# Kernel tuning notes

Hardware: AMD Instinct MI355X
Metric: run time of the kernel (lower is better)

## Reference

```python
import jax, jax.numpy as jnp
import numpy as np

WS = 8            # window_size
SHIFT = WS // 2   # cyclic shift for 'SW' type
HEAD_DIM = 32

def _rel_index(ws):
    # pairwise relative coordinate indices within a window, offset to [0, 2ws-2]
    cord = np.array([[i, j] for i in range(ws) for j in range(ws)])
    rel = cord[:, None, :] - cord[None, :, :] + ws - 1
    return rel[:, :, 0], rel[:, :, 1]

def _shift_mask(h_w, w_w, p):
    # boolean attention mask for shifted windows; True = masked (-inf)
    s = p - SHIFT
    m = np.zeros((h_w, w_w, p, p, p, p), dtype=bool)
    m[-1, :, :s, :, s:, :] = True
    m[-1, :, s:, :, :s, :] = True
    m[:, -1, :, :s, :, s:] = True
    m[:, -1, :, s:, :, :s] = True
    return m.reshape(h_w * w_w, p * p, p * p)

def setup_inputs() -> dict:
    key = jax.random.key(0)
    ks = jax.random.split(key, 6)
    b, H, W, c = 4, 256, 256, 256
    nh = c // HEAD_DIM
    return {
        "x": jax.random.normal(ks[0], (b, H, W, c), jnp.float32),
        "W_qkv": jax.random.normal(ks[1], (c, 3 * c), jnp.float32) * 0.02,
        "b_qkv": jnp.zeros((3 * c,), jnp.float32),
        "rel_pos": jax.random.normal(ks[2], (nh, 2 * WS - 1, 2 * WS - 1), jnp.float32) * 0.02,
        "W_out": jax.random.normal(ks[3], (c, c), jnp.float32) * 0.02,
        "b_out": jnp.zeros((c,), jnp.float32),
    }

def reference(x, W_qkv, b_qkv, rel_pos, W_out, b_out):
    b, H, W, c = x.shape
    nh = c // HEAD_DIM
    scale = HEAD_DIM ** -0.5
    # cyclic shift (type == 'SW')
    x = jnp.roll(x, (-SHIFT, -SHIFT), axis=(1, 2))
    hw, ww = H // WS, W // WS
    nw, p2 = hw * ww, WS * WS
    # partition into windows: [b, nw, p2, c]
    xw = x.reshape(b, hw, WS, ww, WS, c).transpose(0, 1, 3, 2, 4, 5).reshape(b, nw, p2, c)
    # QKV projection; layout of out dim is (3, n_heads, head_dim)
    qkv = (xw @ W_qkv + b_qkv).reshape(b, nw, p2, 3, nh, HEAD_DIM)
    q, k, v = qkv[..., 0, :, :], qkv[..., 1, :, :], qkv[..., 2, :, :]
    # attention scores per head/window: [h, b, nw, p2, p2]
    sim = jnp.einsum('bwphc,bwqhc->hbwpq', q, k) * scale
    ri, rj = _rel_index(WS)
    sim = sim + rel_pos[:, ri, rj][:, None, None]            # relative position bias
    mask = jnp.asarray(_shift_mask(hw, ww, WS))              # [nw, p2, p2]
    sim = jnp.where(mask[None, None], -jnp.inf, sim)
    probs = jax.nn.softmax(sim, axis=-1)
    out = jnp.einsum('hbwpq,bwqhc->bwphc', probs, v).reshape(b, nw, p2, nh * HEAD_DIM)
    out = out @ W_out + b_out
    # un-window: [b, H, W, c_out]
    out = out.reshape(b, hw, ww, WS, WS, -1).transpose(0, 1, 3, 2, 4, 5).reshape(b, H, W, -1)
    return jnp.roll(out, (SHIFT, SHIFT), axis=(1, 2))
```

## Files before the change

kernel.cpp:

```cpp
#include <hip/hip_runtime.h>
#include <hip/hip_bf16.h>

typedef __attribute__((ext_vector_type(4))) float f32x4;
typedef __attribute__((ext_vector_type(2))) unsigned int u32x2;
typedef __attribute__((ext_vector_type(8))) short s16x8;
typedef __attribute__((ext_vector_type(8))) __bf16 bf16v8;
typedef __attribute__((ext_vector_type(8))) _Float16 f16v8;
typedef __attribute__((ext_vector_type(4))) _Float16 f16x4;

#define LDS_XS 0
#define LDS_QS 32768
#define LDS_KS 65536
#define LDS_VT 98304
#define LDS_TOT 131072

__device__ __forceinline__ f32x4 mfma16(s16x8 a, s16x8 b, f32x4 c) {
  return __builtin_amdgcn_mfma_f32_16x16x32_bf16(
      __builtin_bit_cast(bf16v8, a), __builtin_bit_cast(bf16v8, b), c, 0, 0, 0);
}
__device__ __forceinline__ f32x4 mfma16h(s16x8 a, s16x8 b, f32x4 c) {
  return __builtin_amdgcn_mfma_f32_16x16x32_f16(
      __builtin_bit_cast(f16v8, a), __builtin_bit_cast(f16v8, b), c, 0, 0, 0);
}
__device__ __forceinline__ f32x4 mfmah16(f16x4 a, f16x4 b, f32x4 c) {
  return __builtin_amdgcn_mfma_f32_16x16x16f16(a, b, c, 0, 0, 0);
}

__device__ __forceinline__ unsigned int cvt2(float a, float b) {
  __hip_bfloat162 r = __float22bfloat162_rn(make_float2(a, b));
  unsigned int u;
  __builtin_memcpy(&u, &r, 4);
  return u;
}
__device__ __forceinline__ unsigned int cvt2h(float a, float b) {
  auto r = __builtin_amdgcn_cvt_pkrtz(a, b);
  unsigned int u;
  __builtin_memcpy(&u, &r, 4);
  return u;
}
__device__ __forceinline__ f16x4 pack4h(float a, float b, float c, float d) {
  u32x2 u;
  u.x = cvt2h(a, b);
  u.y = cvt2h(c, d);
  f16x4 r;
  __builtin_memcpy(&r, &u, 8);
  return r;
}

__device__ __forceinline__ short f2bf(float f) {
  unsigned u = __float_as_uint(f);
  u += 0x7fffu + ((u >> 16) & 1u);
  return (short)(u >> 16);
}

__device__ __forceinline__ int swz512(int row, int colByte) {
  return row * 512 + (colByte ^ ((row & 7) << 4));
}
__device__ __forceinline__ int swz128(int row, int colByte) {
  return row * 128 + (colByte ^ ((row & 7) << 4));
}

__global__ void prep_w(const float* __restrict__ Wqkv, const float* __restrict__ Wout,
                       const float* __restrict__ relp,
                       short* __restrict__ wqkvT, short* __restrict__ wH,
                       float* __restrict__ relt) {
  int t = blockIdx.x * 256 + threadIdx.x;
  if (t < 768 * 256) {
    int n = t >> 8, k = t & 255;
    wqkvT[t] = f2bf(Wqkv[k * 768 + n]);
  } else if (t < 768 * 256 + 256 * 256) {
    int t2 = t - 768 * 256;
    int n = t2 >> 8, k = t2 & 255;
    _Float16 h = (_Float16)Wout[k * 256 + n];
    unsigned short us;
    __builtin_memcpy(&us, &h, 2);
    wH[t2] = (short)us;
  } else {
    int u = t - 768 * 256 - 256 * 256;
    int r = u & 3, l = (u >> 2) & 63, strip = (u >> 8) & 3;
    int qt = (u >> 10) & 3, h = (u >> 12) & 7, var = (u >> 15) & 3;
    int p = strip * 16 + (l & 15);
    int q = qt * 16 + ((l >> 4) << 2) + r;
    int pi = p >> 3, pj = p & 7, qi = q >> 3, qj = q & 7;
    bool mrow = (var >> 1) & 1, mcol = var & 1;
    bool mk = (mrow && ((pi < 4) != (qi < 4))) || (mcol && ((pj < 4) != (qj < 4)));
    relt[u] = mk ? -1e30f : relp[h * 225 + (pi - qi + 7) * 15 + (pj - qj + 7)];
  }
}

__global__ __launch_bounds__(1024) void swin_mfma(
    const float* __restrict__ x, const float* __restrict__ bqkv,
    const float* __restrict__ bout,
    const short* __restrict__ wqkvT, const short* __restrict__ wH,
    const float* __restrict__ relt, float* __restrict__ out)
{
  __shared__ __align__(16) char lds[LDS_TOT];

  const int tx = threadIdx.x;
  const int w  = tx >> 6;
  const int l  = tx & 63;
  const int g  = l >> 4;
  const int li = l & 15;

  const int b   = blockIdx.x >> 10;
  const int wdw = blockIdx.x & 1023;
  const int wh  = wdw >> 5, wwi = wdw & 31;

  for (int i = 0; i < 4; ++i) {
    int idx = tx + i * 1024;
    int p = idx >> 6, c4 = idx & 63;
    int pi = p >> 3, pj = p & 7;
    int sr = (wh * 8 + pi + 4) & 255;
    int sc = (wwi * 8 + pj + 4) & 255;
    f32x4 v = *(const f32x4*)(x + ((((size_t)b * 256 + sr) * 256 + sc) * 256 + c4 * 4));
    u32x2 uu;
    uu.x = cvt2(v[0], v[1]);
    uu.y = cvt2(v[2], v[3]);
    *(u32x2*)(lds + LDS_XS + swz512(p, c4 * 8)) = uu;
  }
  __syncthreads();

  {
    f32x4 acc[3][4];
    #pragma unroll
    for (int j = 0; j < 3; ++j)
      #pragma unroll
      for (int rb = 0; rb < 4; ++rb)
        acc[j][rb] = (f32x4){0.f, 0.f, 0.f, 0.f};

    int cb[3];
    #pragma unroll
    for (int j = 0; j < 3; ++j) cb[j] = w * 3 + j;

    s16x8 bcur[3], bnext[3];
    #pragma unroll
    for (int j = 0; j < 3; ++j)
      bcur[j] = *(const s16x8*)(wqkvT + (size_t)(cb[j] * 16 + li) * 256 + g * 8);

    #pragma unroll
    for (int kk = 0; kk < 8; ++kk) {
      s16x8 a[4];
      #pragma unroll
      for (int rb = 0; rb < 4; ++rb)
        a[rb] = *(const s16x8*)(lds + LDS_XS + swz512(rb * 16 + li, kk * 64 + g * 16));
      if (kk < 7) {
        #pragma unroll
        for (int j = 0; j < 3; ++j)
          bnext[j] = *(const s16x8*)(wqkvT + (size_t)(cb[j] * 16 + li) * 256
                                     + (kk + 1) * 32 + g * 8);
      }
      #pragma unroll
      for (int j = 0; j < 3; ++j) {
        if (cb[j] < 32)
          #pragma unroll
          for (int rb = 0; rb < 4; ++rb)
            acc[j][rb] = mfma16(bcur[j], a[rb], acc[j][rb]);
        else
          #pragma unroll
          for (int rb = 0; rb < 4; ++rb)
            acc[j][rb] = mfma16(a[rb], bcur[j], acc[j][rb]);
      }
      if (kk < 7) {
        #pragma unroll
        for (int j = 0; j < 3; ++j) bcur[j] = bnext[j];
      }
    }

    #pragma unroll
    for (int j = 0; j < 3; ++j) {
      const int c = cb[j];
      if (c < 16) {
        f32x4 bq = *(const f32x4*)(bqkv + c * 16 + g * 4);
        #pragma unroll
        for (int rb = 0; rb < 4; ++rb) {
          const float SC = 0.17677669529663687f;
          u32x2 uu;
          uu.x = cvt2((acc[j][rb][0] + bq[0]) * SC, (acc[j][rb][1] + bq[1]) * SC);
          uu.y = cvt2((acc[j][rb][2] + bq[2]) * SC, (acc[j][rb][3] + bq[3]) * SC);
          *(u32x2*)(lds + LDS_QS + swz512(rb * 16 + li, c * 32 + g * 8)) = uu;
        }
      } else if (c < 32) {
        f32x4 bk = *(const f32x4*)(bqkv + c * 16 + g * 4);
        #pragma unroll
        for (int rb = 0; rb < 4; ++rb) {
          u32x2 uu;
          uu.x = cvt2(acc[j][rb][0] + bk[0], acc[j][rb][1] + bk[1]);
          uu.y = cvt2(acc[j][rb][2] + bk[2], acc[j][rb][3] + bk[3]);
          *(u32x2*)(lds + LDS_KS + swz512(rb * 16 + li, (c - 16) * 32 + g * 8)) = uu;
        }
      } else {
        const int d = (c - 32) * 16 + li;
        const float bv = bqkv[c * 16 + li];
        #pragma unroll
        for (int rb = 0; rb < 4; ++rb) {
          u32x2 uu;
          uu.x = cvt2h(acc[j][rb][0] + bv, acc[j][rb][1] + bv);
          uu.y = cvt2h(acc[j][rb][2] + bv, acc[j][rb][3] + bv);
          *(u32x2*)(lds + LDS_VT + swz128(d, rb * 32 + g * 8)) = uu;
        }
      }
    }
  }
  __syncthreads();

  {
    const int rvar = ((wh == 31) ? 2 : 0) | ((wwi == 31) ? 1 : 0);
    const int h = w >> 1, phalf = w & 1, p0 = phalf * 32;

    f32x4 rc[2][4];
    #pragma unroll
    for (int pt = 0; pt < 2; ++pt)
      #pragma unroll
      for (int qt = 0; qt < 4; ++qt)
        rc[pt][qt] = *(const f32x4*)(relt
            + ((((rvar * 8 + h) * 4 + qt) * 4 + (phalf * 2 + pt)) * 64 + l) * 4);

    s16x8 qf[2];
    #pragma unroll
    for (int pt = 0; pt < 2; ++pt)
      qf[pt] = *(const s16x8*)(lds + LDS_QS + swz512(p0 + pt * 16 + li, h * 64 + g * 16));
    s16x8 kf[4];
    #pragma unroll
    for (int qt = 0; qt < 4; ++qt)
      kf[qt] = *(const s16x8*)(lds + LDS_KS + swz512(qt * 16 + li, h * 64 + g * 16));
    f16x4 vf[2][4];
    #pragma unroll
    for (int dt = 0; dt < 2; ++dt)
      #pragma unroll
      for (int qt = 0; qt < 4; ++qt)
        vf[dt][qt] = *(const f16x4*)(lds + LDS_VT
                                     + swz128(h * 32 + dt * 16 + li, qt * 32 + g * 8));

    f32x4 simT[2][4];
    #pragma unroll
    for (int pt = 0; pt < 2; ++pt)
      #pragma unroll
      for (int qt = 0; qt < 4; ++qt)
        simT[pt][qt] = mfma16(kf[qt], qf[pt], rc[pt][qt]);

    float rinv[2];
    f16x4 pa[2][4];
    #pragma unroll
    for (int pt = 0; pt < 2; ++pt) {
      float s = 0.f;
      #pragma unroll
      for (int qt = 0; qt < 4; ++qt) {
        float e0 = __expf(simT[pt][qt][0]);
        float e1 = __expf(simT[pt][qt][1]);
        float e2 = __expf(simT[pt][qt][2]);
        float e3 = __expf(simT[pt][qt][3]);
        s += (e0 + e1) + (e2 + e3);
        pa[pt][qt] = pack4h(e0, e1, e2, e3);
      }
      s += __shfl_xor(s, 16);
      s += __shfl_xor(s, 32);
      rinv[pt] = 1.0f / s;
    }

    f32x4 at[2][2];
    #pragma unroll
    for (int pt = 0; pt < 2; ++pt)
      #pragma unroll
      for (int dt = 0; dt < 2; ++dt)
        at[pt][dt] = (f32x4){0.f, 0.f, 0.f, 0.f};
    #pragma unroll
    for (int qt = 0; qt < 4; ++qt)
      #pragma unroll
      for (int pt = 0; pt < 2; ++pt)
        #pragma unroll
        for (int dt = 0; dt < 2; ++dt)
          at[pt][dt] = mfmah16(vf[dt][qt], pa[pt][qt], at[pt][dt]);

    #pragma unroll
    for (int pt = 0; pt < 2; ++pt)
      #pragma unroll
      for (int dt = 0; dt < 2; ++dt) {
        const f32x4 a4 = at[pt][dt];
        u32x2 hh;
        hh.x = cvt2h(a4[0] * rinv[pt], a4[1] * rinv[pt]);
        hh.y = cvt2h(a4[2] * rinv[pt], a4[3] * rinv[pt]);
        *(u32x2*)(lds + LDS_XS + swz512(p0 + pt * 16 + li, h * 64 + dt * 32 + g * 8)) = hh;
      }
  }
  __syncthreads();

  {
    f32x4 acc2[4];
    #pragma unroll
    for (int rb = 0; rb < 4; ++rb)
      acc2[rb] = (f32x4){0.f, 0.f, 0.f, 0.f};

    s16x8 bc = *(const s16x8*)(wH + (size_t)(w * 16 + li) * 256 + g * 8);
    s16x8 bn;

    #pragma unroll
    for (int kk = 0; kk < 8; ++kk) {
      s16x8 a[4];
      #pragma unroll
      for (int rb = 0; rb < 4; ++rb)
        a[rb] = *(const s16x8*)(lds + LDS_XS + swz512(rb * 16 + li, kk * 64 + g * 16));
      if (kk < 7)
        bn = *(const s16x8*)(wH + (size_t)(w * 16 + li) * 256 + (kk + 1) * 32 + g * 8);
      #pragma unroll
      for (int rb = 0; rb < 4; ++rb)
        acc2[rb] = mfma16h(a[rb], bc, acc2[rb]);
      if (kk < 7) bc = bn;
    }

    const int n = w * 16 + li;
    const float bo = bout[n];
    #pragma unroll
    for (int rb = 0; rb < 4; ++rb)
      #pragma unroll
      for (int r = 0; r < 4; ++r) {
        int m = rb * 16 + g * 4 + r;
        int pi = m >> 3, pj = m & 7;
        int dr = (wh * 8 + pi + 4) & 255;
        int dc = (wwi * 8 + pj + 4) & 255;
        out[(((size_t)b * 256 + dr) * 256 + dc) * 256 + n] = acc2[rb][r] + bo;
      }
  }
}

extern "C" void kernel_launch(void* const* d_in, const int* in_sizes, int n_in,
                              void* d_out, int out_size, void* d_ws, size_t ws_size,
                              hipStream_t stream) {
  (void)in_sizes; (void)n_in; (void)out_size; (void)ws_size;
  const float* x    = (const float*)d_in[0];
  const float* Wqkv = (const float*)d_in[1];
  const float* bqkv = (const float*)d_in[2];
  const float* relp = (const float*)d_in[3];
  const float* Wout = (const float*)d_in[4];
  const float* bout = (const float*)d_in[5];
  float* out = (float*)d_out;

  short* wqkvT = (short*)d_ws;
  short* wH    = wqkvT + 768 * 256;
  float* relt  = (float*)(wH + 256 * 256);

  hipLaunchKernelGGL(prep_w, dim3(1536), dim3(256), 0, stream,
                     Wqkv, Wout, relp, wqkvT, wH, relt);
  hipLaunchKernelGGL(swin_mfma, dim3(4096), dim3(1024), 0, stream,
                     x, bqkv, bout, wqkvT, wH, relt, out);
}
```

Measured before the change: 457.8 us.

## Halve block size to 512 threads and double per-wave work in all phases

```diff
diff --git a/kernel.cpp b/kernel.cpp
--- a/kernel.cpp
+++ b/kernel.cpp
@@ -88,7 +88,7 @@
   }
 }
 
-__global__ __launch_bounds__(1024) void swin_mfma(
+__global__ __launch_bounds__(512, 2) void swin_mfma(
     const float* __restrict__ x, const float* __restrict__ bqkv,
     const float* __restrict__ bout,
     const short* __restrict__ wqkvT, const short* __restrict__ wH,
@@ -106,8 +106,8 @@
   const int wdw = blockIdx.x & 1023;
   const int wh  = wdw >> 5, wwi = wdw & 31;
 
-  for (int i = 0; i < 4; ++i) {
-    int idx = tx + i * 1024;
+  for (int i = 0; i < 8; ++i) {
+    int idx = tx + i * 512;
     int p = idx >> 6, c4 = idx & 63;
     int pi = p >> 3, pj = p & 7;
     int sr = (wh * 8 + pi + 4) & 255;
@@ -121,21 +121,23 @@
   __syncthreads();
 
   {
-    f32x4 acc[3][4];
-    #pragma unroll
-    for (int j = 0; j < 3; ++j)
+    f32x4 acc[6][4];
+    #pragma unroll
+    for (int j = 0; j < 6; ++j)
       #pragma unroll
       for (int rb = 0; rb < 4; ++rb)
         acc[j][rb] = (f32x4){0.f, 0.f, 0.f, 0.f};
 
-    int cb[3];
-    #pragma unroll
-    for (int j = 0; j < 3; ++j) cb[j] = w * 3 + j;
-
-    s16x8 bcur[3], bnext[3];
-    #pragma unroll
-    for (int j = 0; j < 3; ++j)
-      bcur[j] = *(const s16x8*)(wqkvT + (size_t)(cb[j] * 16 + li) * 256 + g * 8);
+    int ocol[6];
+    #pragma unroll
+    for (int j = 0; j < 4; ++j) ocol[j] = (w * 4 + j) * 16 + li;
+    #pragma unroll
+    for (int j = 4; j < 6; ++j) ocol[j] = 512 + (w * 2 + (j - 4)) * 16 + li;
+
+    s16x8 bcur[6], bnext[6];
+    #pragma unroll
+    for (int j = 0; j < 6; ++j)
+      bcur[j] = *(const s16x8*)(wqkvT + (size_t)ocol[j] * 256 + g * 8);
 
     #pragma unroll
     for (int kk = 0; kk < 8; ++kk) {
@@ -145,59 +147,59 @@
         a[rb] = *(const s16x8*)(lds + LDS_XS + swz512(rb * 16 + li, kk * 64 + g * 16));
       if (kk < 7) {
         #pragma unroll
-        for (int j = 0; j < 3; ++j)
-          bnext[j] = *(const s16x8*)(wqkvT + (size_t)(cb[j] * 16 + li) * 256
-                                     + (kk + 1) * 32 + g * 8);
-      }
-      #pragma unroll
-      for (int j = 0; j < 3; ++j) {
-        if (cb[j] < 32)
-          #pragma unroll
-          for (int rb = 0; rb < 4; ++rb)
-            acc[j][rb] = mfma16(bcur[j], a[rb], acc[j][rb]);
-        else
-          #pragma unroll
-          for (int rb = 0; rb < 4; ++rb)
-            acc[j][rb] = mfma16(a[rb], bcur[j], acc[j][rb]);
-      }
+        for (int j = 0; j < 6; ++j)
+          bnext[j] = *(const s16x8*)(wqkvT + (size_t)ocol[j] * 256 + (kk + 1) * 32 + g * 8);
+      }
+      #pragma unroll
+      for (int j = 0; j < 4; ++j)
+        #pragma unroll
+        for (int rb = 0; rb < 4; ++rb)
+          acc[j][rb] = mfma16(bcur[j], a[rb], acc[j][rb]);
+      #pragma unroll
+      for (int j = 4; j < 6; ++j)
+        #pragma unroll
+        for (int rb = 0; rb < 4; ++rb)
+          acc[j][rb] = mfma16(a[rb], bcur[j], acc[j][rb]);
       if (kk < 7) {
         #pragma unroll
-        for (int j = 0; j < 3; ++j) bcur[j] = bnext[j];
-      }
-    }
-
-    #pragma unroll
-    for (int j = 0; j < 3; ++j) {
-      const int c = cb[j];
-      if (c < 16) {
-        f32x4 bq = *(const f32x4*)(bqkv + c * 16 + g * 4);
+        for (int j = 0; j < 6; ++j) bcur[j] = bnext[j];
+      }
+    }
+
+    #pragma unroll
+    for (int j = 0; j < 4; ++j) {
+      const int cb = w * 4 + j;
+      if (cb < 16) {
+        f32x4 bq = *(const f32x4*)(bqkv + cb * 16 + g * 4);
         #pragma unroll
         for (int rb = 0; rb < 4; ++rb) {
           const float SC = 0.17677669529663687f;
           u32x2 uu;
           uu.x = cvt2((acc[j][rb][0] + bq[0]) * SC, (acc[j][rb][1] + bq[1]) * SC);
           uu.y = cvt2((acc[j][rb][2] + bq[2]) * SC, (acc[j][rb][3] + bq[3]) * SC);
-          *(u32x2*)(lds + LDS_QS + swz512(rb * 16 + li, c * 32 + g * 8)) = uu;
-        }
-      } else if (c < 32) {
-        f32x4 bk = *(const f32x4*)(bqkv + c * 16 + g * 4);
+          *(u32x2*)(lds + LDS_QS + swz512(rb * 16 + li, cb * 32 + g * 8)) = uu;
+        }
+      } else {
+        f32x4 bk = *(const f32x4*)(bqkv + cb * 16 + g * 4);
         #pragma unroll
         for (int rb = 0; rb < 4; ++rb) {
           u32x2 uu;
           uu.x = cvt2(acc[j][rb][0] + bk[0], acc[j][rb][1] + bk[1]);
           uu.y = cvt2(acc[j][rb][2] + bk[2], acc[j][rb][3] + bk[3]);
-          *(u32x2*)(lds + LDS_KS + swz512(rb * 16 + li, (c - 16) * 32 + g * 8)) = uu;
-        }
-      } else {
-        const int d = (c - 32) * 16 + li;
-        const float bv = bqkv[c * 16 + li];
-        #pragma unroll
-        for (int rb = 0; rb < 4; ++rb) {
-          u32x2 uu;
-          uu.x = cvt2h(acc[j][rb][0] + bv, acc[j][rb][1] + bv);
-          uu.y = cvt2h(acc[j][rb][2] + bv, acc[j][rb][3] + bv);
-          *(u32x2*)(lds + LDS_VT + swz128(d, rb * 32 + g * 8)) = uu;
-        }
+          *(u32x2*)(lds + LDS_KS + swz512(rb * 16 + li, (cb - 16) * 32 + g * 8)) = uu;
+        }
+      }
+    }
+    #pragma unroll
+    for (int j = 4; j < 6; ++j) {
+      const int d = (w * 2 + (j - 4)) * 16 + li;
+      const float bv = bqkv[512 + d];
+      #pragma unroll
+      for (int rb = 0; rb < 4; ++rb) {
+        u32x2 uu;
+        uu.x = cvt2h(acc[j][rb][0] + bv, acc[j][rb][1] + bv);
+        uu.y = cvt2h(acc[j][rb][2] + bv, acc[j][rb][3] + bv);
+        *(u32x2*)(lds + LDS_VT + swz128(d, rb * 32 + g * 8)) = uu;
       }
     }
   }
@@ -205,93 +207,102 @@
 
   {
     const int rvar = ((wh == 31) ? 2 : 0) | ((wwi == 31) ? 1 : 0);
-    const int h = w >> 1, phalf = w & 1, p0 = phalf * 32;
-
-    f32x4 rc[2][4];
-    #pragma unroll
-    for (int pt = 0; pt < 2; ++pt)
+    const int phalf = w & 1, p0 = phalf * 32;
+
+    #pragma unroll 1
+    for (int iter = 0; iter < 2; ++iter) {
+      const int h = (w >> 1) + iter * 4;
+
+      f32x4 rc[2][4];
+      #pragma unroll
+      for (int pt = 0; pt < 2; ++pt)
+        #pragma unroll
+        for (int qt = 0; qt < 4; ++qt)
+          rc[pt][qt] = *(const f32x4*)(relt
+              + ((((rvar * 8 + h) * 4 + qt) * 4 + (phalf * 2 + pt)) * 64 + l) * 4);
+
+      s16x8 qf[2];
+      #pragma unroll
+      for (int pt = 0; pt < 2; ++pt)
+        qf[pt] = *(const s16x8*)(lds + LDS_QS + swz512(p0 + pt * 16 + li, h * 64 + g * 16));
+      s16x8 kf[4];
       #pragma unroll
       for (int qt = 0; qt < 4; ++qt)
-        rc[pt][qt] = *(const f32x4*)(relt
-            + ((((rvar * 8 + h) * 4 + qt) * 4 + (phalf * 2 + pt)) * 64 + l) * 4);
-
-    s16x8 qf[2];
-    #pragma unroll
-    for (int pt = 0; pt < 2; ++pt)
-      qf[pt] = *(const s16x8*)(lds + LDS_QS + swz512(p0 + pt * 16 + li, h * 64 + g * 16));
-    s16x8 kf[4];
-    #pragma unroll
-    for (int qt = 0; qt < 4; ++qt)
-      kf[qt] = *(const s16x8*)(lds + LDS_KS + swz512(qt * 16 + li, h * 64 + g * 16));
-    f16x4 vf[2][4];
-    #pragma unroll
-    for (int dt = 0; dt < 2; ++dt)
+        kf[qt] = *(const s16x8*)(lds + LDS_KS + swz512(qt * 16 + li, h * 64 + g * 16));
+      f16x4 vf[2][4];
+      #pragma unroll
+      for (int dt = 0; dt < 2; ++dt)
+        #pragma unroll
+        for (int qt = 0; qt < 4; ++qt)
+          vf[dt][qt] = *(const f16x4*)(lds + LDS_VT
+                                       + swz128(h * 32 + dt * 16 + li, qt * 32 + g * 8));
+
+      f32x4 simT[2][4];
+      #pragma unroll
+      for (int pt = 0; pt < 2; ++pt)
+        #pragma unroll
+        for (int qt = 0; qt < 4; ++qt)
+          simT[pt][qt] = mfma16(kf[qt], qf[pt], rc[pt][qt]);
+
+      float rinv[2];
+      f16x4 pa[2][4];
+      #pragma unroll
+      for (int pt = 0; pt < 2; ++pt) {
+        float s = 0.f;
+        #pragma unroll
+        for (int qt = 0; qt < 4; ++qt) {
+          float e0 = __expf(simT[pt][qt][0]);
+          float e1 = __expf(simT[pt][qt][1]);
+          float e2 = __expf(simT[pt][qt][2]);
+          float e3 = __expf(simT[pt][qt][3]);
+          s += (e0 + e1) + (e2 + e3);
+          pa[pt][qt] = pack4h(e0, e1, e2, e3);
+        }
+        s += __shfl_xor(s, 16);
+        s += __shfl_xor(s, 32);
+        rinv[pt] = 1.0f / s;
+      }
+
+      f32x4 at[2][2];
+      #pragma unroll
+      for (int pt = 0; pt < 2; ++pt)
+        #pragma unroll
+        for (int dt = 0; dt < 2; ++dt)
+          at[pt][dt] = (f32x4){0.f, 0.f, 0.f, 0.f};
       #pragma unroll
       for (int qt = 0; qt < 4; ++qt)
-        vf[dt][qt] = *(const f16x4*)(lds + LDS_VT
-                                     + swz128(h * 32 + dt * 16 + li, qt * 32 + g * 8));
-
-    f32x4 simT[2][4];
-    #pragma unroll
-    for (int pt = 0; pt < 2; ++pt)
-      #pragma unroll
-      for (int qt = 0; qt < 4; ++qt)
-        simT[pt][qt] = mfma16(kf[qt], qf[pt], rc[pt][qt]);
-
-    float rinv[2];
-    f16x4 pa[2][4];
-    #pragma unroll
-    for (int pt = 0; pt < 2; ++pt) {
-      float s = 0.f;
-      #pragma unroll
-      for (int qt = 0; qt < 4; ++qt) {
-        float e0 = __expf(simT[pt][qt][0]);
-        float e1 = __expf(simT[pt][qt][1]);
-        float e2 = __expf(simT[pt][qt][2]);
-        float e3 = __expf(simT[pt][qt][3]);
-        s += (e0 + e1) + (e2 + e3);
-        pa[pt][qt] = pack4h(e0, e1, e2, e3);
-      }
-      s += __shfl_xor(s, 16);
-      s += __shfl_xor(s, 32);
-      rinv[pt] = 1.0f / s;
-    }
-
-    f32x4 at[2][2];
-    #pragma unroll
-    for (int pt = 0; pt < 2; ++pt)
-      #pragma unroll
-      for (int dt = 0; dt < 2; ++dt)
-        at[pt][dt] = (f32x4){0.f, 0.f, 0.f, 0.f};
-    #pragma unroll
-    for (int qt = 0; qt < 4; ++qt)
-      #pragma unroll
-      for (int pt = 0; pt < 2; ++pt)
-        #pragma unroll
-        for (int dt = 0; dt < 2; ++dt)
-          at[pt][dt] = mfmah16(vf[dt][qt], pa[pt][qt], at[pt][dt]);
-
-    #pragma unroll
-    for (int pt = 0; pt < 2; ++pt)
-      #pragma unroll
-      for (int dt = 0; dt < 2; ++dt) {
-        const f32x4 a4 = at[pt][dt];
-        u32x2 hh;
-        hh.x = cvt2h(a4[0] * rinv[pt], a4[1] * rinv[pt]);
-        hh.y = cvt2h(a4[2] * rinv[pt], a4[3] * rinv[pt]);
-        *(u32x2*)(lds + LDS_XS + swz512(p0 + pt * 16 + li, h * 64 + dt * 32 + g * 8)) = hh;
-      }
+        #pragma unroll
+        for (int pt = 0; pt < 2; ++pt)
+          #pragma unroll
+          for (int dt = 0; dt < 2; ++dt)
+            at[pt][dt] = mfmah16(vf[dt][qt], pa[pt][qt], at[pt][dt]);
+
+      #pragma unroll
+      for (int pt = 0; pt < 2; ++pt)
+        #pragma unroll
+        for (int dt = 0; dt < 2; ++dt) {
+          const f32x4 a4 = at[pt][dt];
+          u32x2 hh;
+          hh.x = cvt2h(a4[0] * rinv[pt], a4[1] * rinv[pt]);
+          hh.y = cvt2h(a4[2] * rinv[pt], a4[3] * rinv[pt]);
+          *(u32x2*)(lds + LDS_XS + swz512(p0 + pt * 16 + li, h * 64 + dt * 32 + g * 8)) = hh;
+        }
+    }
   }
   __syncthreads();
 
   {
-    f32x4 acc2[4];
-    #pragma unroll
-    for (int rb = 0; rb < 4; ++rb)
-      acc2[rb] = (f32x4){0.f, 0.f, 0.f, 0.f};
-
-    s16x8 bc = *(const s16x8*)(wH + (size_t)(w * 16 + li) * 256 + g * 8);
-    s16x8 bn;
+    f32x4 acc2[2][4];
+    #pragma unroll
+    for (int c = 0; c < 2; ++c)
+      #pragma unroll
+      for (int rb = 0; rb < 4; ++rb)
+        acc2[c][rb] = (f32x4){0.f, 0.f, 0.f, 0.f};
+
+    s16x8 bc[2], bn[2];
+    #pragma unroll
+    for (int c = 0; c < 2; ++c)
+      bc[c] = *(const s16x8*)(wH + (size_t)((w * 2 + c) * 16 + li) * 256 + g * 8);
 
     #pragma unroll
     for (int kk = 0; kk < 8; ++kk) {
@@ -299,26 +310,38 @@
       #pragma unroll
       for (int rb = 0; rb < 4; ++rb)
         a[rb] = *(const s16x8*)(lds + LDS_XS + swz512(rb * 16 + li, kk * 64 + g * 16));
-      if (kk < 7)
-        bn = *(const s16x8*)(wH + (size_t)(w * 16 + li) * 256 + (kk + 1) * 32 + g * 8);
-      #pragma unroll
-      for (int rb = 0; rb < 4; ++rb)
-        acc2[rb] = mfma16h(a[rb], bc, acc2[rb]);
-      if (kk < 7) bc = bn;
-    }
-
-    const int n = w * 16 + li;
-    const float bo = bout[n];
-    #pragma unroll
-    for (int rb = 0; rb < 4; ++rb)
-      #pragma unroll
-      for (int r = 0; r < 4; ++r) {
-        int m = rb * 16 + g * 4 + r;
-        int pi = m >> 3, pj = m & 7;
-        int dr = (wh * 8 + pi + 4) & 255;
-        int dc = (wwi * 8 + pj + 4) & 255;
-        out[(((size_t)b * 256 + dr) * 256 + dc) * 256 + n] = acc2[rb][r] + bo;
-      }
+      if (kk < 7) {
+        #pragma unroll
+        for (int c = 0; c < 2; ++c)
+          bn[c] = *(const s16x8*)(wH + (size_t)((w * 2 + c) * 16 + li) * 256
+                                  + (kk + 1) * 32 + g * 8);
+      }
+      #pragma unroll
+      for (int c = 0; c < 2; ++c)
+        #pragma unroll
+        for (int rb = 0; rb < 4; ++rb)
+          acc2[c][rb] = mfma16h(a[rb], bc[c], acc2[c][rb]);
+      if (kk < 7) {
+        #pragma unroll
+        for (int c = 0; c < 2; ++c) bc[c] = bn[c];
+      }
+    }
+
+    #pragma unroll
+    for (int c = 0; c < 2; ++c) {
+      const int n = (w * 2 + c) * 16 + li;
+      const float bo = bout[n];
+      #pragma unroll
+      for (int rb = 0; rb < 4; ++rb)
+        #pragma unroll
+        for (int r = 0; r < 4; ++r) {
+          int m = rb * 16 + g * 4 + r;
+          int pi = m >> 3, pj = m & 7;
+          int dr = (wh * 8 + pi + 4) & 255;
+          int dc = (wwi * 8 + pj + 4) & 255;
+          out[(((size_t)b * 256 + dr) * 256 + dc) * 256 + n] = acc2[c][rb][r] + bo;
+        }
+    }
   }
 }
 
@@ -340,6 +363,6 @@
 
   hipLaunchKernelGGL(prep_w, dim3(1536), dim3(256), 0, stream,
                      Wqkv, Wout, relp, wqkvT, wH, relt);
-  hipLaunchKernelGGL(swin_mfma, dim3(4096), dim3(1024), 0, stream,
+  hipLaunchKernelGGL(swin_mfma, dim3(4096), dim3(512), 0, stream,
                      x, bqkv, bout, wqkvT, wH, relt, out);
 }
```

Measured after the change: 401.5 us. 1.14x faster.
